# Performance work log

Hardware: AMD Instinct MI355X
Metric: run time of the kernel (lower is better)

## Reference

```python
import jax, jax.numpy as jnp
import numpy as np

D = 1024
H = 16
FF = 4 * D


def layer_norm(x, g, b, eps=1e-5):
    mu = jnp.mean(x, axis=-1, keepdims=True)
    var = jnp.var(x, axis=-1, keepdims=True)
    return (x - mu) * jax.lax.rsqrt(var + eps) * g + b


def setup_inputs() -> dict:
    key = jax.random.key(0)
    ks = jax.random.split(key, 8)
    s = lambda fan_in: 1.0 / np.sqrt(fan_in)
    return {
        "x": jax.random.normal(ks[0], (2, 2048, D), dtype=jnp.float32),
        "ln1_g": jnp.ones((D,), jnp.float32),
        "ln1_b": jnp.zeros((D,), jnp.float32),
        "w_qkv": jax.random.uniform(ks[1], (D, 3 * D), jnp.float32, -s(D), s(D)),
        "b_qkv": jnp.zeros((3 * D,), jnp.float32),
        "w_out": jax.random.uniform(ks[2], (D, D), jnp.float32, -s(D), s(D)),
        "b_out": jnp.zeros((D,), jnp.float32),
        "ln2_g": jnp.ones((D,), jnp.float32),
        "ln2_b": jnp.zeros((D,), jnp.float32),
        "w_fc1": jax.random.uniform(ks[3], (D, FF), jnp.float32, -s(D), s(D)),
        "b_fc1": jnp.zeros((FF,), jnp.float32),
        "w_fc2": jax.random.uniform(ks[4], (FF, D), jnp.float32, -s(FF), s(FF)),
        "b_fc2": jnp.zeros((D,), jnp.float32),
    }


def reference(x, ln1_g, ln1_b, w_qkv, b_qkv, w_out, b_out,
              ln2_g, ln2_b, w_fc1, b_fc1, w_fc2, b_fc2):
    b, n, c = x.shape
    hd = c // H
    scale = hd ** -0.5

    # --- pre-norm MHA ---
    h = layer_norm(x, ln1_g, ln1_b)
    qkv = h @ w_qkv + b_qkv                      # [b,n,3c]
    qkv = qkv.reshape(b, n, 3, H, hd)
    q = jnp.transpose(qkv[:, :, 0], (0, 2, 1, 3))  # [b,H,n,hd]
    k = jnp.transpose(qkv[:, :, 1], (0, 2, 1, 3))
    v = jnp.transpose(qkv[:, :, 2], (0, 2, 1, 3))
    attn = jnp.einsum('bhqd,bhkd->bhqk', q, k) * scale
    attn = jax.nn.softmax(attn, axis=-1)
    o = jnp.einsum('bhqk,bhkd->bhqd', attn, v)   # [b,H,n,hd]
    o = jnp.transpose(o, (0, 2, 1, 3)).reshape(b, n, c)
    x = x + (o @ w_out + b_out)

    # --- pre-norm FFN ---
    h = layer_norm(x, ln2_g, ln2_b)
    h = jax.nn.gelu(h @ w_fc1 + b_fc1, approximate=False)
    x = x + (h @ w_fc2 + b_fc2)
    return x
```

## Files before the change

kernel.cpp:

```cpp
#include <hip/hip_runtime.h>
#include <stdint.h>
#include <math.h>

#define D_MODEL 1024
#define NHEAD   16
#define HDIM    64
#define FFDIM   4096
#define SEQ     2048
#define BATCH   2
#define NTOK    (BATCH*SEQ)
#define QKVN    (3*D_MODEL)

typedef __bf16 bf16;
typedef __attribute__((ext_vector_type(8))) __bf16 bf16x8;
typedef __attribute__((ext_vector_type(4))) __bf16 bf16x4;
typedef __attribute__((ext_vector_type(4))) float f32x4;

__device__ __forceinline__ void gld_lds16(const void* g, void* l) {
    __builtin_amdgcn_global_load_lds((__attribute__((address_space(1))) void*)g,
                                     (__attribute__((address_space(3))) void*)l,
                                     16, 0, 0);
}

__device__ __forceinline__ float fast_exp2(float x) {
#if __has_builtin(__builtin_amdgcn_exp2f)
    return __builtin_amdgcn_exp2f(x);
#else
    return __expf(x * 0.69314718056f);
#endif
}

__global__ __launch_bounds__(256)
void k_transpose_all(const float* __restrict__ w_qkv, const float* __restrict__ w_out,
                     const float* __restrict__ w_fc1, const float* __restrict__ w_fc2,
                     bf16* __restrict__ t_qkv, bf16* __restrict__ t_out,
                     bf16* __restrict__ t_fc1, bf16* __restrict__ t_fc2) {
    __shared__ float tile[32][33];
    int bid = blockIdx.x;
    const float* W; bf16* Wt; int K, N, ti;
    if (bid < 3072)       { W = w_qkv; Wt = t_qkv; K = 1024; N = 3072; ti = bid; }
    else if (bid < 4096)  { W = w_out; Wt = t_out; K = 1024; N = 1024; ti = bid - 3072; }
    else if (bid < 8192)  { W = w_fc1; Wt = t_fc1; K = 1024; N = 4096; ti = bid - 4096; }
    else                  { W = w_fc2; Wt = t_fc2; K = 4096; N = 1024; ti = bid - 8192; }
    int tn = N >> 5;
    int n0 = (ti % tn) * 32, k0 = (ti / tn) * 32;
    int tx = threadIdx.x, ty = threadIdx.y;
#pragma unroll
    for (int i = 0; i < 4; i++)
        tile[ty + i * 8][tx] = W[(size_t)(k0 + ty + i * 8) * N + n0 + tx];
    __syncthreads();
#pragma unroll
    for (int i = 0; i < 4; i++)
        Wt[(size_t)(n0 + ty + i * 8) * K + k0 + tx] = (bf16)tile[tx][ty + i * 8];
}

__global__ __launch_bounds__(256)
void k_vtrans(const bf16* __restrict__ qkv, bf16* __restrict__ vT) {
    __shared__ bf16 t[32][33];
    int tok0 = blockIdx.x * 32, f0 = blockIdx.y * 32;
    int tx = threadIdx.x, ty = threadIdx.y;
#pragma unroll
    for (int i = 0; i < 4; i++)
        t[ty + i * 8][tx] = qkv[(size_t)(tok0 + ty + i * 8) * QKVN + 2 * D_MODEL + f0 + tx];
    __syncthreads();
    int s = tx;
    int pp = (s < 16) ? ((s >> 2) * 8 + (s & 3))
                      : (((s - 16) >> 2) * 8 + ((s - 16) & 3) + 4);
#pragma unroll
    for (int i = 0; i < 4; i++)
        vT[(size_t)(f0 + ty + i * 8) * NTOK + tok0 + pp] = t[tx][ty + i * 8];
}

__global__ __launch_bounds__(256)
void k_layernorm(const float* __restrict__ x, const float* __restrict__ g,
                 const float* __restrict__ b, bf16* __restrict__ out) {
    int row = blockIdx.x;
    int tid = threadIdx.x;
    float4 v = ((const float4*)(x + (size_t)row * D_MODEL))[tid];
    float s  = v.x + v.y + v.z + v.w;
    float ss = v.x * v.x + v.y * v.y + v.z * v.z + v.w * v.w;
#pragma unroll
    for (int off = 32; off > 0; off >>= 1) {
        s  += __shfl_down(s, off, 64);
        ss += __shfl_down(ss, off, 64);
    }
    __shared__ float red[2][4];
    __shared__ float mv[2];
    int wave = tid >> 6, lane = tid & 63;
    if (lane == 0) { red[0][wave] = s; red[1][wave] = ss; }
    __syncthreads();
    if (tid == 0) {
        float S  = red[0][0] + red[0][1] + red[0][2] + red[0][3];
        float SS = red[1][0] + red[1][1] + red[1][2] + red[1][3];
        float mu = S * (1.0f / D_MODEL);
        float var = SS * (1.0f / D_MODEL) - mu * mu;
        mv[0] = mu;
        mv[1] = rsqrtf(var + 1e-5f);
    }
    __syncthreads();
    float mu = mv[0], rs = mv[1];
    float4 gv = ((const float4*)g)[tid];
    float4 bv = ((const float4*)b)[tid];
    bf16x4 ov = { (bf16)((v.x - mu) * rs * gv.x + bv.x),
                  (bf16)((v.y - mu) * rs * gv.y + bv.y),
                  (bf16)((v.z - mu) * rs * gv.z + bv.z),
                  (bf16)((v.w - mu) * rs * gv.w + bv.w) };
    *(bf16x4*)(out + (size_t)row * D_MODEL + tid * 4) = ov;
}

template <int DO_GELU, int DO_RES, int OUT_BF16, int BN>
__global__ __launch_bounds__(256)
void k_gemm(const bf16* __restrict__ A, const bf16* __restrict__ Bt,
            const float* __restrict__ bias, const float* __restrict__ res,
            float* __restrict__ outf, bf16* __restrict__ outb,
            int M, int N, int K) {
    constexpr int WN = BN / 32;
    __shared__ bf16 As[2][128 * 32];
    __shared__ bf16 Bs[2][BN * 32];
    int tid  = threadIdx.x;
    int wave = tid >> 6, lane = tid & 63;
    int quad = lane >> 4, l16 = lane & 15;
    int m0 = blockIdx.y * 128, n0 = blockIdx.x * BN;
    int wm = (wave >> 1) * 64, wn = (wave & 1) * (BN / 2);

    f32x4 acc[4][WN];
#pragma unroll
    for (int i = 0; i < 4; i++)
#pragma unroll
        for (int j = 0; j < WN; j++) acc[i][j] = (f32x4){0.f, 0.f, 0.f, 0.f};

    int lrow = lane >> 2;
    int lcol = (lane & 3) * 8;
    const bf16* gA0 = A + (size_t)(m0 + wave * 32 + lrow) * K + lcol;
    const bf16* gA1 = gA0 + (size_t)16 * K;
    const bf16* gB0;
    const bf16* gB1 = nullptr;
    if constexpr (BN == 128) {
        gB0 = Bt + (size_t)(n0 + wave * 32 + lrow) * K + lcol;
        gB1 = gB0 + (size_t)16 * K;
    } else {
        gB0 = Bt + (size_t)(n0 + wave * 16 + lrow) * K + lcol;
    }

    int wA0 = wave * 1024 + lane * 8;
    int wA1 = wA0 + 512;
    int wB0 = (BN == 128) ? (wave * 1024 + lane * 8) : (wave * 512 + lane * 8);
    int wB1 = wB0 + 512;

    {
        bf16x8 rA0 = *(const bf16x8*)(gA0);
        bf16x8 rA1 = *(const bf16x8*)(gA1);
        bf16x8 rB0 = *(const bf16x8*)(gB0);
        bf16x8 rB1;
        if constexpr (BN == 128) rB1 = *(const bf16x8*)(gB1);
        *(bf16x8*)(&As[0][wA0]) = rA0;
        *(bf16x8*)(&As[0][wA1]) = rA1;
        *(bf16x8*)(&Bs[0][wB0]) = rB0;
        if constexpr (BN == 128) *(bf16x8*)(&Bs[0][wB1]) = rB1;
    }
    __syncthreads();

    const bf16* curA = &As[0][0];
    const bf16* curB = &Bs[0][0];
    bf16* nxtA = &As[1][0];
    bf16* nxtB = &Bs[1][0];

    int niter = K / 32;
    for (int t = 1; t < niter; t++) {
        int k0 = t * 32;
        bf16x8 rA0 = *(const bf16x8*)(gA0 + k0);
        bf16x8 rA1 = *(const bf16x8*)(gA1 + k0);
        bf16x8 rB0 = *(const bf16x8*)(gB0 + k0);
        bf16x8 rB1;
        if constexpr (BN == 128) rB1 = *(const bf16x8*)(gB1 + k0);

        bf16x8 af[4], bfr[WN];
#pragma unroll
        for (int mi = 0; mi < 4; mi++)
            af[mi] = *(const bf16x8*)(curA + (wm + mi * 16 + l16) * 32 + quad * 8);
#pragma unroll
        for (int ni = 0; ni < WN; ni++)
            bfr[ni] = *(const bf16x8*)(curB + (wn + ni * 16 + l16) * 32 + quad * 8);
#pragma unroll
        for (int mi = 0; mi < 4; mi++)
#pragma unroll
            for (int ni = 0; ni < WN; ni++)
                acc[mi][ni] = __builtin_amdgcn_mfma_f32_16x16x32_bf16(af[mi], bfr[ni], acc[mi][ni], 0, 0, 0);

        *(bf16x8*)(nxtA + wA0) = rA0;
        *(bf16x8*)(nxtA + wA1) = rA1;
        *(bf16x8*)(nxtB + wB0) = rB0;
        if constexpr (BN == 128) *(bf16x8*)(nxtB + wB1) = rB1;
        __syncthreads();

        const bf16* tA = curA; curA = nxtA; nxtA = (bf16*)tA;
        const bf16* tB = curB; curB = nxtB; nxtB = (bf16*)tB;
    }

    {
        bf16x8 af[4], bfr[WN];
#pragma unroll
        for (int mi = 0; mi < 4; mi++)
            af[mi] = *(const bf16x8*)(curA + (wm + mi * 16 + l16) * 32 + quad * 8);
#pragma unroll
        for (int ni = 0; ni < WN; ni++)
            bfr[ni] = *(const bf16x8*)(curB + (wn + ni * 16 + l16) * 32 + quad * 8);
#pragma unroll
        for (int mi = 0; mi < 4; mi++)
#pragma unroll
            for (int ni = 0; ni < WN; ni++)
                acc[mi][ni] = __builtin_amdgcn_mfma_f32_16x16x32_bf16(af[mi], bfr[ni], acc[mi][ni], 0, 0, 0);
    }

#pragma unroll
    for (int mi = 0; mi < 4; mi++) {
        int row = m0 + wm + mi * 16 + quad * 4;
#pragma unroll
        for (int ni = 0; ni < WN; ni++) {
            int col = n0 + wn + ni * 16 + l16;
            float bb = bias[col];
#pragma unroll
            for (int r = 0; r < 4; r++) {
                float v = acc[mi][ni][r] + bb;
                if (DO_GELU) v = 0.5f * v * (1.0f + erff(v * 0.70710678118f));
                size_t idx = (size_t)(row + r) * N + col;
                if (DO_RES) v += res[idx];
                if (OUT_BF16) outb[idx] = (bf16)v;
                else          outf[idx] = v;
            }
        }
    }
}

__global__ __launch_bounds__(256)
void k_attention2(const bf16* __restrict__ qkv, const bf16* __restrict__ vT,
                  bf16* __restrict__ o) {
    __shared__ bf16 Ks[2][64][32];
    __shared__ bf16 Vs[2][64][32];

    int tid = threadIdx.x, wave = tid >> 6, lane = tid & 63;
    int quad = lane >> 4, l16 = lane & 15;
    int bh = blockIdx.y;
    int b = bh >> 4, h = bh & 15;
    int q0 = blockIdx.x * 64 + wave * 16;

    const bf16* Qb  = qkv + (size_t)b * SEQ * QKVN + h * HDIM;
    const bf16* Kb  = Qb + D_MODEL;
    const bf16* vTb = vT + (size_t)h * HDIM * NTOK + b * SEQ;

    const float QSCALE = 0.125f * 1.44269504089f;
    bf16x8 qf[2];
#pragma unroll
    for (int c = 0; c < 2; c++) {
        bf16x8 qraw = *(const bf16x8*)(Qb + (size_t)(q0 + l16) * QKVN + c * 32 + quad * 8);
#pragma unroll
        for (int i = 0; i < 8; i++) qf[c][i] = (bf16)((float)qraw[i] * QSCALE);
    }

    const bf16* gK0 = Kb + (size_t)(wave * 16 + (lane >> 2)) * QKVN + 0 * 32 + (lane & 3) * 8;
    const bf16* gK1 = gK0 + 32;
    const bf16* gV0 = vTb + (size_t)(wave * 16 + (lane >> 2)) * NTOK + (lane & 3) * 8;
    const bf16* gV1 = gV0 + 32;
    bf16* lK0 = &Ks[0][wave * 16][0];
    bf16* lK1 = &Ks[1][wave * 16][0];
    bf16* lV0 = &Vs[0][wave * 16][0];
    bf16* lV1 = &Vs[1][wave * 16][0];

    f32x4 oacc[4];
#pragma unroll
    for (int i = 0; i < 4; i++) oacc[i] = (f32x4){0.f, 0.f, 0.f, 0.f};
    float lsum = 0.f;

    for (int kv0 = 0; kv0 < SEQ; kv0 += 64) {
        __syncthreads();
        size_t koff = (size_t)kv0 * QKVN;
        gld_lds16(gK0 + koff, lK0);
        gld_lds16(gK1 + koff, lK1);
        gld_lds16(gV0 + kv0, lV0);
        gld_lds16(gV1 + kv0, lV1);
        __syncthreads();

        f32x4 s[4];
#pragma unroll
        for (int t = 0; t < 4; t++) {
            bf16x8 af0 = *(const bf16x8*)(&Ks[0][t * 16 + l16][quad * 8]);
            bf16x8 af1 = *(const bf16x8*)(&Ks[1][t * 16 + l16][quad * 8]);
            f32x4 z = (f32x4){0.f, 0.f, 0.f, 0.f};
            z = __builtin_amdgcn_mfma_f32_16x16x32_bf16(af0, qf[0], z, 0, 0, 0);
            z = __builtin_amdgcn_mfma_f32_16x16x32_bf16(af1, qf[1], z, 0, 0, 0);
            s[t] = z;
        }

        bf16x4 p[4];
#pragma unroll
        for (int t = 0; t < 4; t++)
#pragma unroll
            for (int r = 0; r < 4; r++) {
                float pf = fast_exp2(s[t][r]);
                lsum += pf;
                p[t][r] = (bf16)pf;
            }

#pragma unroll
        for (int tp = 0; tp < 2; tp++) {
            bf16x8 pa = __builtin_shufflevector(p[2 * tp], p[2 * tp + 1], 0, 1, 2, 3, 4, 5, 6, 7);
#pragma unroll
            for (int nt = 0; nt < 4; nt++) {
                bf16x8 vb = *(const bf16x8*)(&Vs[tp][nt * 16 + l16][quad * 8]);
                oacc[nt] = __builtin_amdgcn_mfma_f32_16x16x32_bf16(pa, vb, oacc[nt], 0, 0, 0);
            }
        }
    }

    lsum += __shfl_xor(lsum, 16, 64);
    lsum += __shfl_xor(lsum, 32, 64);
    float invl[4];
#pragma unroll
    for (int r = 0; r < 4; r++)
        invl[r] = 1.0f / __shfl(lsum, quad * 4 + r, 16);

#pragma unroll
    for (int nt = 0; nt < 4; nt++)
#pragma unroll
        for (int r = 0; r < 4; r++)
            o[(size_t)(b * SEQ + q0 + quad * 4 + r) * D_MODEL + h * HDIM + nt * 16 + l16] =
                (bf16)(oacc[nt][r] * invl[r]);
}

extern "C" void kernel_launch(void* const* d_in, const int* in_sizes, int n_in,
                              void* d_out, int out_size, void* d_ws, size_t ws_size,
                              hipStream_t stream) {
    const float* x     = (const float*)d_in[0];
    const float* ln1_g = (const float*)d_in[1];
    const float* ln1_b = (const float*)d_in[2];
    const float* w_qkv = (const float*)d_in[3];
    const float* b_qkv = (const float*)d_in[4];
    const float* w_out = (const float*)d_in[5];
    const float* b_out = (const float*)d_in[6];
    const float* ln2_g = (const float*)d_in[7];
    const float* ln2_b = (const float*)d_in[8];
    const float* w_fc1 = (const float*)d_in[9];
    const float* b_fc1 = (const float*)d_in[10];
    const float* w_fc2 = (const float*)d_in[11];
    const float* b_fc2 = (const float*)d_in[12];
    float* out = (float*)d_out;

    uintptr_t ws = (uintptr_t)d_ws;
    bf16* wt_qkv = (bf16*)(ws + 0);
    bf16* wt_out = (bf16*)(ws + 6291456);
    bf16* wt_fc1 = (bf16*)(ws + 8388608);
    bf16* wt_fc2 = (bf16*)(ws + 16777216);
    bf16* hbuf   = (bf16*)(ws + 25165824);
    bf16* vT     = hbuf;
    bf16* qkv    = (bf16*)(ws + 33554432);
    bf16* attn_o = (bf16*)(ws + 58720256);
    bf16* hgelu  = (bf16*)(ws + 33554432);

    k_transpose_all<<<12288, dim3(32, 8), 0, stream>>>(w_qkv, w_out, w_fc1, w_fc2,
                                                       wt_qkv, wt_out, wt_fc1, wt_fc2);

    k_layernorm<<<NTOK, 256, 0, stream>>>(x, ln1_g, ln1_b, hbuf);

    k_gemm<0, 0, 1, 128><<<dim3(QKVN / 128, NTOK / 128), 256, 0, stream>>>(
        hbuf, wt_qkv, b_qkv, nullptr, nullptr, qkv, NTOK, QKVN, D_MODEL);

    k_vtrans<<<dim3(NTOK / 32, D_MODEL / 32), dim3(32, 8), 0, stream>>>(qkv, vT);

    k_attention2<<<dim3(SEQ / 64, BATCH * NHEAD), 256, 0, stream>>>(qkv, vT, attn_o);

    k_gemm<0, 1, 0, 64><<<dim3(D_MODEL / 64, NTOK / 128), 256, 0, stream>>>(
        attn_o, wt_out, b_out, x, out, nullptr, NTOK, D_MODEL, D_MODEL);

    k_layernorm<<<NTOK, 256, 0, stream>>>(out, ln2_g, ln2_b, hbuf);

    k_gemm<1, 0, 1, 128><<<dim3(FFDIM / 128, NTOK / 128), 256, 0, stream>>>(
        hbuf, wt_fc1, b_fc1, nullptr, nullptr, hgelu, NTOK, FFDIM, D_MODEL);

    k_gemm<0, 1, 0, 64><<<dim3(D_MODEL / 64, NTOK / 128), 256, 0, stream>>>(
        hgelu, wt_fc2, b_fc2, out, out, nullptr, NTOK, D_MODEL, FFDIM);
}
```

Baseline: 377.3 us.

## Add register double-buffered GEMM pipeline, XCD-aware block swizzle, and split-K for FC2

After: 367.6 us. -2.6%, faster.

```diff
diff --git a/kernel.cpp b/kernel.cpp
--- a/kernel.cpp
+++ b/kernel.cpp
@@ -29,6 +29,12 @@
     return __expf(x * 0.69314718056f);
 #endif
 }
+
+#define GEMM_BAR() do {                                        \
+    asm volatile("s_waitcnt lgkmcnt(0)" ::: "memory");         \
+    __builtin_amdgcn_s_barrier();                              \
+    asm volatile("" ::: "memory");                             \
+} while (0)
 
 __global__ __launch_bounds__(256)
 void k_transpose_all(const float* __restrict__ w_qkv, const float* __restrict__ w_out,
@@ -108,20 +114,28 @@
     *(bf16x4*)(out + (size_t)row * D_MODEL + tid * 4) = ov;
 }
 
-template <int DO_GELU, int DO_RES, int OUT_BF16, int BN>
+template <int DO_GELU, int DO_RES, int OUT_BF16, int BN, int PIPE2, int SPLITK>
 __global__ __launch_bounds__(256)
 void k_gemm(const bf16* __restrict__ A, const bf16* __restrict__ Bt,
             const float* __restrict__ bias, const float* __restrict__ res,
             float* __restrict__ outf, bf16* __restrict__ outb,
-            int M, int N, int K) {
+            float* __restrict__ part, int M, int N, int K) {
     constexpr int WN = BN / 32;
     __shared__ bf16 As[2][128 * 32];
     __shared__ bf16 Bs[2][BN * 32];
     int tid  = threadIdx.x;
     int wave = tid >> 6, lane = tid & 63;
     int quad = lane >> 4, l16 = lane & 15;
-    int m0 = blockIdx.y * 128, n0 = blockIdx.x * BN;
+
+    int nwg = gridDim.x * gridDim.y;
+    int bid = blockIdx.y * gridDim.x + blockIdx.x;
+    int sid = (bid & 7) * (nwg >> 3) + (bid >> 3);
+    int bx = sid % gridDim.x, by = sid / gridDim.x;
+    int m0 = by * 128, n0 = bx * BN;
     int wm = (wave >> 1) * 64, wn = (wave & 1) * (BN / 2);
+
+    int Keff = (SPLITK == 2) ? (K >> 1) : K;
+    int koff = (SPLITK == 2) ? blockIdx.z * Keff : 0;
 
     f32x4 acc[4][WN];
 #pragma unroll
@@ -131,15 +145,15 @@
 
     int lrow = lane >> 2;
     int lcol = (lane & 3) * 8;
-    const bf16* gA0 = A + (size_t)(m0 + wave * 32 + lrow) * K + lcol;
+    const bf16* gA0 = A + (size_t)(m0 + wave * 32 + lrow) * K + koff + lcol;
     const bf16* gA1 = gA0 + (size_t)16 * K;
     const bf16* gB0;
     const bf16* gB1 = nullptr;
     if constexpr (BN == 128) {
-        gB0 = Bt + (size_t)(n0 + wave * 32 + lrow) * K + lcol;
+        gB0 = Bt + (size_t)(n0 + wave * 32 + lrow) * K + koff + lcol;
         gB1 = gB0 + (size_t)16 * K;
     } else {
-        gB0 = Bt + (size_t)(n0 + wave * 16 + lrow) * K + lcol;
+        gB0 = Bt + (size_t)(n0 + wave * 16 + lrow) * K + koff + lcol;
     }
 
     int wA0 = wave * 1024 + lane * 8;
@@ -147,69 +161,66 @@
     int wB0 = (BN == 128) ? (wave * 1024 + lane * 8) : (wave * 512 + lane * 8);
     int wB1 = wB0 + 512;
 
-    {
-        bf16x8 rA0 = *(const bf16x8*)(gA0);
-        bf16x8 rA1 = *(const bf16x8*)(gA1);
-        bf16x8 rB0 = *(const bf16x8*)(gB0);
-        bf16x8 rB1;
-        if constexpr (BN == 128) rB1 = *(const bf16x8*)(gB1);
-        *(bf16x8*)(&As[0][wA0]) = rA0;
-        *(bf16x8*)(&As[0][wA1]) = rA1;
-        *(bf16x8*)(&Bs[0][wB0]) = rB0;
-        if constexpr (BN == 128) *(bf16x8*)(&Bs[0][wB1]) = rB1;
-    }
-    __syncthreads();
-
-    const bf16* curA = &As[0][0];
-    const bf16* curB = &Bs[0][0];
-    bf16* nxtA = &As[1][0];
-    bf16* nxtB = &Bs[1][0];
-
-    int niter = K / 32;
-    for (int t = 1; t < niter; t++) {
-        int k0 = t * 32;
-        bf16x8 rA0 = *(const bf16x8*)(gA0 + k0);
-        bf16x8 rA1 = *(const bf16x8*)(gA1 + k0);
-        bf16x8 rB0 = *(const bf16x8*)(gB0 + k0);
-        bf16x8 rB1;
-        if constexpr (BN == 128) rB1 = *(const bf16x8*)(gB1 + k0);
-
+    auto issue = [&](bf16x8* r, int k0) {
+        r[0] = *(const bf16x8*)(gA0 + k0);
+        r[1] = *(const bf16x8*)(gA1 + k0);
+        r[2] = *(const bf16x8*)(gB0 + k0);
+        if constexpr (BN == 128) r[3] = *(const bf16x8*)(gB1 + k0);
+    };
+    auto commit = [&](int buf, const bf16x8* r) {
+        *(bf16x8*)(&As[buf][wA0]) = r[0];
+        *(bf16x8*)(&As[buf][wA1]) = r[1];
+        *(bf16x8*)(&Bs[buf][wB0]) = r[2];
+        if constexpr (BN == 128) *(bf16x8*)(&Bs[buf][wB1]) = r[3];
+    };
+    auto compute = [&](int buf) {
         bf16x8 af[4], bfr[WN];
 #pragma unroll
         for (int mi = 0; mi < 4; mi++)
-            af[mi] = *(const bf16x8*)(curA + (wm + mi * 16 + l16) * 32 + quad * 8);
+            af[mi] = *(const bf16x8*)(&As[buf][(wm + mi * 16 + l16) * 32 + quad * 8]);
 #pragma unroll
         for (int ni = 0; ni < WN; ni++)
-            bfr[ni] = *(const bf16x8*)(curB + (wn + ni * 16 + l16) * 32 + quad * 8);
+            bfr[ni] = *(const bf16x8*)(&Bs[buf][(wn + ni * 16 + l16) * 32 + quad * 8]);
 #pragma unroll
         for (int mi = 0; mi < 4; mi++)
 #pragma unroll
             for (int ni = 0; ni < WN; ni++)
                 acc[mi][ni] = __builtin_amdgcn_mfma_f32_16x16x32_bf16(af[mi], bfr[ni], acc[mi][ni], 0, 0, 0);
-
-        *(bf16x8*)(nxtA + wA0) = rA0;
-        *(bf16x8*)(nxtA + wA1) = rA1;
-        *(bf16x8*)(nxtB + wB0) = rB0;
-        if constexpr (BN == 128) *(bf16x8*)(nxtB + wB1) = rB1;
+    };
+
+    int niter = Keff / 32;
+    bf16x8 r0[4], r1[4];
+
+    if constexpr (!PIPE2) {
+        issue(r0, 0);
+        commit(0, r0);
         __syncthreads();
-
-        const bf16* tA = curA; curA = nxtA; nxtA = (bf16*)tA;
-        const bf16* tB = curB; curB = nxtB; nxtB = (bf16*)tB;
-    }
-
-    {
-        bf16x8 af[4], bfr[WN];
-#pragma unroll
-        for (int mi = 0; mi < 4; mi++)
-            af[mi] = *(const bf16x8*)(curA + (wm + mi * 16 + l16) * 32 + quad * 8);
-#pragma unroll
-        for (int ni = 0; ni < WN; ni++)
-            bfr[ni] = *(const bf16x8*)(curB + (wn + ni * 16 + l16) * 32 + quad * 8);
-#pragma unroll
-        for (int mi = 0; mi < 4; mi++)
-#pragma unroll
-            for (int ni = 0; ni < WN; ni++)
-                acc[mi][ni] = __builtin_amdgcn_mfma_f32_16x16x32_bf16(af[mi], bfr[ni], acc[mi][ni], 0, 0, 0);
+        for (int t = 1; t < niter; t++) {
+            issue(r0, t * 32);
+            compute((t - 1) & 1);
+            commit(t & 1, r0);
+            __syncthreads();
+        }
+        compute((niter - 1) & 1);
+    } else {
+        issue(r0, 0);
+        commit(0, r0);
+        issue(r1, 32);
+        GEMM_BAR();
+        for (int t = 1; t + 2 < niter; t += 2) {
+            issue(r0, (t + 1) * 32);
+            compute(0);
+            commit(1, r1);
+            GEMM_BAR();
+            issue(r1, (t + 2) * 32);
+            compute(1);
+            commit(0, r0);
+            GEMM_BAR();
+        }
+        compute(0);
+        commit(1, r1);
+        GEMM_BAR();
+        compute(1);
     }
 
 #pragma unroll
@@ -218,6 +229,14 @@
 #pragma unroll
         for (int ni = 0; ni < WN; ni++) {
             int col = n0 + wn + ni * 16 + l16;
+            if constexpr (SPLITK == 2) {
+                if (blockIdx.z == 1) {
+#pragma unroll
+                    for (int r = 0; r < 4; r++)
+                        part[(size_t)(row + r) * N + col] = acc[mi][ni][r];
+                    continue;
+                }
+            }
             float bb = bias[col];
 #pragma unroll
             for (int r = 0; r < 4; r++) {
@@ -230,6 +249,16 @@
             }
         }
     }
+}
+
+__global__ __launch_bounds__(256)
+void k_add(float* __restrict__ out, const float* __restrict__ part) {
+    size_t i = (size_t)blockIdx.x * 256 + threadIdx.x;
+    float4* o = (float4*)out;
+    const float4* p = (const float4*)part;
+    float4 a = o[i], q = p[i];
+    a.x += q.x; a.y += q.y; a.z += q.z; a.w += q.w;
+    o[i] = a;
 }
 
 __global__ __launch_bounds__(256)
@@ -355,27 +384,30 @@
     bf16* qkv    = (bf16*)(ws + 33554432);
     bf16* attn_o = (bf16*)(ws + 58720256);
     bf16* hgelu  = (bf16*)(ws + 33554432);
+    float* fc2p  = (float*)(ws + 0);
 
     k_transpose_all<<<12288, dim3(32, 8), 0, stream>>>(w_qkv, w_out, w_fc1, w_fc2,
                                                        wt_qkv, wt_out, wt_fc1, wt_fc2);
 
     k_layernorm<<<NTOK, 256, 0, stream>>>(x, ln1_g, ln1_b, hbuf);
 
-    k_gemm<0, 0, 1, 128><<<dim3(QKVN / 128, NTOK / 128), 256, 0, stream>>>(
-        hbuf, wt_qkv, b_qkv, nullptr, nullptr, qkv, NTOK, QKVN, D_MODEL);
+    k_gemm<0, 0, 1, 128, 0, 1><<<dim3(QKVN / 128, NTOK / 128), 256, 0, stream>>>(
+        hbuf, wt_qkv, b_qkv, nullptr, nullptr, qkv, nullptr, NTOK, QKVN, D_MODEL);
 
     k_vtrans<<<dim3(NTOK / 32, D_MODEL / 32), dim3(32, 8), 0, stream>>>(qkv, vT);
 
     k_attention2<<<dim3(SEQ / 64, BATCH * NHEAD), 256, 0, stream>>>(qkv, vT, attn_o);
 
-    k_gemm<0, 1, 0, 64><<<dim3(D_MODEL / 64, NTOK / 128), 256, 0, stream>>>(
-        attn_o, wt_out, b_out, x, out, nullptr, NTOK, D_MODEL, D_MODEL);
+    k_gemm<0, 1, 0, 64, 1, 1><<<dim3(D_MODEL / 64, NTOK / 128), 256, 0, stream>>>(
+        attn_o, wt_out, b_out, x, out, nullptr, nullptr, NTOK, D_MODEL, D_MODEL);
 
     k_layernorm<<<NTOK, 256, 0, stream>>>(out, ln2_g, ln2_b, hbuf);
 
-    k_gemm<1, 0, 1, 128><<<dim3(FFDIM / 128, NTOK / 128), 256, 0, stream>>>(
-        hbuf, wt_fc1, b_fc1, nullptr, nullptr, hgelu, NTOK, FFDIM, D_MODEL);
-
-    k_gemm<0, 1, 0, 64><<<dim3(D_MODEL / 64, NTOK / 128), 256, 0, stream>>>(
-        hgelu, wt_fc2, b_fc2, out, out, nullptr, NTOK, D_MODEL, FFDIM);
-}
+    k_gemm<1, 0, 1, 128, 0, 1><<<dim3(FFDIM / 128, NTOK / 128), 256, 0, stream>>>(
+        hbuf, wt_fc1, b_fc1, nullptr, nullptr, hgelu, nullptr, NTOK, FFDIM, D_MODEL);
+
+    k_gemm<0, 1, 0, 128, 1, 2><<<dim3(D_MODEL / 128, NTOK / 128, 2), 256, 0, stream>>>(
+        hgelu, wt_fc2, b_fc2, out, out, nullptr, fc2p, NTOK, D_MODEL, FFDIM);
+
+    k_add<<<(NTOK * D_MODEL / 4) / 256, 256, 0, stream>>>(out, fc2p);
+}
```
